# Kernel optimization log

Measured on AMD Instinct MI355X. Metric: run time of the kernel, lower is better.

The kernel has to match this reference:

```python
import jax, jax.numpy as jnp
import numpy as np

HIDDEN = 1024
INTER = 4096
N_EXPERTS = 8


def geglu(x, w1, w2, w3):
    # x: [N, C], w1/w2: [C, I], w3: [I, C]
    return (jax.nn.gelu(x @ w1, approximate=False) * (x @ w2)) @ w3


def setup_inputs() -> dict:
    key = jax.random.key(0)
    ks = jax.random.split(key, 8)
    s = 0.02
    x = jax.random.normal(ks[0], (2, 2048, HIDDEN), dtype=jnp.float32)
    w1s = jax.random.normal(ks[1], (HIDDEN, INTER), dtype=jnp.float32) * s
    w2s = jax.random.normal(ks[2], (HIDDEN, INTER), dtype=jnp.float32) * s
    w3s = jax.random.normal(ks[3], (INTER, HIDDEN), dtype=jnp.float32) * s
    W1 = jax.random.normal(ks[4], (N_EXPERTS, HIDDEN, INTER), dtype=jnp.float32) * s
    W2 = jax.random.normal(ks[5], (N_EXPERTS, HIDDEN, INTER), dtype=jnp.float32) * s
    W3 = jax.random.normal(ks[6], (N_EXPERTS, INTER, HIDDEN), dtype=jnp.float32) * s
    Wg = jax.random.normal(ks[7], (HIDDEN, N_EXPERTS), dtype=jnp.float32) * s
    return {"x": x, "w1s": w1s, "w2s": w2s, "w3s": w3s,
            "W1": W1, "W2": W2, "W3": W3, "Wg": Wg}


def reference(x, w1s, w2s, w3s, W1, W2, W3, Wg):
    B, T, C = x.shape
    xf = x.reshape(-1, C)  # [N, C]
    shared = geglu(xf, w1s, w2s, w3s)  # [N, C]
    logits = xf @ Wg  # [N, E]
    # top-1 of softmax == argmax of logits (softmax is monotone);
    # NOTE: original torch code does NOT multiply by the routing prob.
    idx = jnp.argmax(logits, axis=-1)  # [N]
    final = jnp.zeros_like(xf)
    for e in range(N_EXPERTS):  # small fixed expert count
        y = geglu(xf, W1[e], W2[e], W3[e])  # [N, C]
        final = final + jnp.where((idx == e)[:, None], y, 0.0)
    return (shared + final).reshape(B, T, C)
```

## Files before the change

### kernel.cpp

```cpp
#include <hip/hip_runtime.h>
#include <stdint.h>

#define HIDDEN 1024
#define INTER  4096
#define NTOK   4096
#define HROWS  (2*NTOK)
#define MAXB1  40
#define MAXB2  72
#define NMAT   27

typedef unsigned short u16;
typedef unsigned int   u32;
typedef __bf16  bf16x8 __attribute__((ext_vector_type(8)));
typedef float   f32x4  __attribute__((ext_vector_type(4)));
typedef u32     u32x4  __attribute__((ext_vector_type(4)));

#define WAITVM(N) asm volatile("s_waitcnt vmcnt(" #N ")" ::: "memory")

__device__ __forceinline__ void hard_barrier() {
  asm volatile("" ::: "memory");
  __builtin_amdgcn_s_barrier();
  asm volatile("" ::: "memory");
}

__device__ __forceinline__ u16 f2bf(float f) {
  u32 u = __float_as_uint(f);
  u32 r = u + 0x7FFFu + ((u >> 16) & 1u);
  return (u16)(r >> 16);
}

__device__ __forceinline__ u32 cvt_pk_bf16(float lo, float hi) {
  u32 r;
  asm("v_cvt_pk_bf16_f32 %0, %1, %2" : "=v"(r) : "v"(lo), "v"(hi));
  return r;
}

__device__ __forceinline__ void glds16(const void* g, void* l) {
  __builtin_amdgcn_global_load_lds(
      (const __attribute__((address_space(1))) void*)g,
      (__attribute__((address_space(3))) void*)l, 16, 0, 0);
}


__global__ void k_init(int* cnt, int* fill) {
  if (threadIdx.x < 8) { cnt[threadIdx.x] = 0; fill[threadIdx.x] = 0; }
}

__global__ __launch_bounds__(256) void k_gate(const float* __restrict__ x,
                                              const float* __restrict__ wg,
                                              int* __restrict__ idx,
                                              int* __restrict__ cnt) {
  int wave = threadIdx.x >> 6, lane = threadIdx.x & 63;
  int t = blockIdx.x * 4 + wave;
  if (t >= NTOK) return;
  float acc[8];
  #pragma unroll
  for (int e = 0; e < 8; ++e) acc[e] = 0.f;
  const float* xr = x + (size_t)t * HIDDEN;
  for (int c = lane; c < HIDDEN; c += 64) {
    float xv = xr[c];
    const float* wrow = wg + (size_t)c * 8;
    #pragma unroll
    for (int e = 0; e < 8; ++e) acc[e] += xv * wrow[e];
  }
  #pragma unroll
  for (int e = 0; e < 8; ++e)
    for (int s = 32; s; s >>= 1) acc[e] += __shfl_xor(acc[e], s);
  if (lane == 0) {
    int best = 0; float bv = acc[0];
    #pragma unroll
    for (int e = 1; e < 8; ++e) if (acc[e] > bv) { bv = acc[e]; best = e; }
    idx[t] = best;
    atomicAdd(&cnt[best], 1);
  }
}

__global__ void k_cvt(const float* __restrict__ x, u16* __restrict__ xb, int n4) {
  int i = blockIdx.x * blockDim.x + threadIdx.x;
  if (i >= n4) return;
  float4 v = ((const float4*)x)[i];
  ushort4 o;
  o.x = f2bf(v.x); o.y = f2bf(v.y); o.z = f2bf(v.z); o.w = f2bf(v.w);
  ((ushort4*)xb)[i] = o;
}

__global__ void k_table(const int* __restrict__ cnt, int* __restrict__ off,
                        int4* __restrict__ tab1, int* __restrict__ nblk1,
                        int4* __restrict__ tab2, int* __restrict__ nblk2) {
  if (threadIdx.x != 0 || blockIdx.x != 0) return;
  int o = 0;
  int offs[8];
  for (int e = 0; e < 8; ++e) { offs[e] = o; off[e] = o; o += cnt[e]; }
  int nb = 0;
  for (int m = 0; m < NTOK / 256; ++m)
    tab1[nb++] = make_int4(8, m * 256, 256, 0);
  for (int e = 0; e < 8; ++e)
    for (int j = 0; j * 256 < cnt[e]; ++j) {
      int rows = cnt[e] - j * 256; if (rows > 256) rows = 256;
      tab1[nb++] = make_int4(e, NTOK + offs[e] + j * 256, rows, offs[e] + j * 256);
    }
  *nblk1 = nb;
  nb = 0;
  for (int m = 0; m < NTOK / 128; ++m)
    tab2[nb++] = make_int4(8, m * 128, 128, 0);
  for (int e = 0; e < 8; ++e)
    for (int j = 0; j * 128 < cnt[e]; ++j) {
      int rows = cnt[e] - j * 128; if (rows > 128) rows = 128;
      tab2[nb++] = make_int4(e, NTOK + offs[e] + j * 128, rows, offs[e] + j * 128);
    }
  *nblk2 = nb;
}

__global__ void k_scatter(const int* __restrict__ idx, const int* __restrict__ off,
                          int* __restrict__ fill, int* __restrict__ perm) {
  int t = blockIdx.x * blockDim.x + threadIdx.x;
  if (t >= NTOK) return;
  int e = idx[t];
  int p = atomicAdd(&fill[e], 1);
  perm[off[e] + p] = t;
}


__global__ __launch_bounds__(256) void k_wcvt(
    const float* __restrict__ w1s, const float* __restrict__ w2s,
    const float* __restrict__ w3s, const float* __restrict__ W1,
    const float* __restrict__ W2,  const float* __restrict__ W3,
    u16* __restrict__ Wb)
{
  int bid = blockIdx.x;
  int m = bid >> 9, pair = bid & 511;
  const float* src; int N, Tp, kt, pp2;
  if (m < 18) {
    N = INTER; Tp = 32;
    int mm = (m < 9) ? m : m - 9;
    const float* sp = (m < 9) ? w1s : w2s;
    const float* ep = (m < 9) ? W1 : W2;
    src = (mm == 0) ? sp : ep + (size_t)(mm - 1) * HIDDEN * INTER;
    kt = pair >> 4; pp2 = pair & 15;
  } else {
    N = HIDDEN; Tp = 8;
    int mm = m - 18;
    src = (mm == 0) ? w3s : W3 + (size_t)(mm - 1) * INTER * HIDDEN;
    kt = pair >> 2; pp2 = pair & 3;
  }

  __shared__ float tileF[32 * 256];
  int tid = threadIdx.x;
  const float* in0 = src + (size_t)(kt * 32) * N + pp2 * 256;
  #pragma unroll
  for (int i = 0; i < 8; ++i) {
    int f = tid + 256 * i;
    int k = f >> 6, c4 = f & 63;
    *(float4*)&tileF[k * 256 + c4 * 4] = *(const float4*)(in0 + (size_t)k * N + c4 * 4);
  }
  __syncthreads();

  int p2 = tid >> 7, n = tid & 127;
  u16* outp = Wb + ((size_t)m * 1024 + kt * Tp + pp2 * 2 + p2) * 4096 + n * 32;
  #pragma unroll
  for (int s = 0; s < 4; ++s) {
    int k8 = s ^ ((n >> 1) & 3);
    const float* col = &tileF[(k8 * 8) * 256 + p2 * 128 + n];
    u32x4 pk;
    pk.x = cvt_pk_bf16(col[0],    col[256]);
    pk.y = cvt_pk_bf16(col[512],  col[768]);
    pk.z = cvt_pk_bf16(col[1024], col[1280]);
    pk.w = cvt_pk_bf16(col[1536], col[1792]);
    *(u32x4*)(outp + s * 8) = pk;
  }
}


__global__ __launch_bounds__(512, 2) void k_mlp1(
    const u16* __restrict__ xb, const u16* __restrict__ Wb,
    const int* __restrict__ perm, const int4* __restrict__ tab,
    const int* __restrict__ nblk, u16* __restrict__ Hbuf)
{
  int bx = blockIdx.x;
  if (bx >= *nblk) return;
  int4 te = tab[bx];
  int g = te.x, hrow0 = te.y, rows = te.z, pb = te.w;
  int m1 = (g == 8) ? 0 : 1 + g;
  int pp = blockIdx.y;
  int nbase = pp * 128;

  extern __shared__ __align__(16) char smem[];
  int tid = threadIdx.x;
  int w = tid >> 6, lane = tid & 63;
  int q = lane >> 4, rl = lane & 15;
  int mw = w >> 2, nw = w & 3;

  int tokj[2];
  #pragma unroll
  for (int j = 0; j < 2; ++j) {
    int r = w * 32 + j * 16 + (lane >> 2);
    int rc = (r < rows) ? r : (rows - 1);
    tokj[j] = (g == 8) ? (hrow0 + rc) : perm[pb + rc];
  }
  int gch = ((lane & 3) ^ ((lane >> 3) & 3)) * 16;

  const char* pB1 = (const char*)Wb + ((size_t)m1 * 1024 + pp) * 8192;
  const char* pB2 = (const char*)Wb + ((size_t)(m1 + 9) * 1024 + pp) * 8192;

  f32x4 acc1[8][2], acc2[8][2];
  f32x4 z = {0.f, 0.f, 0.f, 0.f};
  #pragma unroll
  for (int mi = 0; mi < 8; ++mi)
    #pragma unroll
    for (int ni = 0; ni < 2; ++ni) { acc1[mi][ni] = z; acc2[mi][ni] = z; }

  auto STAGE = [&](int t) {
    char* L = smem + (t & 3) * 32768;
    int k0 = t * 32;
    #pragma unroll
    for (int j = 0; j < 2; ++j) {
      const char* src = (const char*)xb + ((size_t)tokj[j] * HIDDEN + k0) * 2 + gch;
      glds16(src, L + w * 2048 + j * 1024);
    }
    glds16(pB1 + (size_t)t * 262144 + (tid << 4), L + 16384 + w * 1024);
    glds16(pB2 + (size_t)t * 262144 + (tid << 4), L + 24576 + w * 1024);
  };

  int co = (q ^ ((rl >> 1) & 3)) * 8;

  auto COMPUTE = [&](int t) {
    const u16* LA  = (const u16*)(smem + (t & 3) * 32768);
    const u16* LB1 = LA + 8192;
    const u16* LB2 = LA + 12288;
    bf16x8 af[8], b1[2], b2[2];
    #pragma unroll
    for (int mi = 0; mi < 8; ++mi)
      af[mi] = *(const bf16x8*)&LA[(mw * 128 + mi * 16 + rl) * 32 + co];
    #pragma unroll
    for (int ni = 0; ni < 2; ++ni) {
      int n = nw * 32 + ni * 16 + rl;
      b1[ni] = *(const bf16x8*)&LB1[n * 32 + co];
      b2[ni] = *(const bf16x8*)&LB2[n * 32 + co];
    }
    __builtin_amdgcn_s_setprio(1);
    #pragma unroll
    for (int mi = 0; mi < 8; ++mi)
      #pragma unroll
      for (int ni = 0; ni < 2; ++ni) {
        acc1[mi][ni] = __builtin_amdgcn_mfma_f32_16x16x32_bf16(af[mi], b1[ni], acc1[mi][ni], 0, 0, 0);
        acc2[mi][ni] = __builtin_amdgcn_mfma_f32_16x16x32_bf16(af[mi], b2[ni], acc2[mi][ni], 0, 0, 0);
      }
    __builtin_amdgcn_s_setprio(0);
  };

  const int NT = HIDDEN / 32;
  STAGE(0); STAGE(1); STAGE(2);
  for (int t = 0; t < NT; ++t) {
    if (t + 3 < NT) STAGE(t + 3);
    int rem = NT - 1 - t;
    if (rem >= 3)      WAITVM(12);
    else if (rem == 2) WAITVM(8);
    else if (rem == 1) WAITVM(4);
    else               WAITVM(0);
    hard_barrier();
    COMPUTE(t);
    hard_barrier();
  }

  #pragma unroll
  for (int mi = 0; mi < 8; ++mi) {
    #pragma unroll
    for (int j = 0; j < 4; ++j) {
      int r = mw * 128 + mi * 16 + q * 4 + j;
      if (r < rows) {
        size_t hb = (size_t)(hrow0 + r) * INTER + nbase + nw * 32;
        #pragma unroll
        for (int ni = 0; ni < 2; ++ni) {
          float h1 = acc1[mi][ni][j];
          float h2 = acc2[mi][ni][j];
          float ge = 0.5f * h1 * (1.0f + erff(h1 * 0.7071067811865476f));
          Hbuf[hb + ni * 16 + rl] = f2bf(ge * h2);
        }
      }
    }
  }
}


__global__ __launch_bounds__(512, 2) void k_mlp2(
    const u16* __restrict__ Hbuf, const u16* __restrict__ Wb,
    const int* __restrict__ perm, const int4* __restrict__ tab,
    const int* __restrict__ nblk, float* __restrict__ out,
    float* __restrict__ yexp)
{
  int bx = blockIdx.x;
  if (bx >= *nblk) return;
  int4 te = tab[bx];
  int g = te.x, hrow0 = te.y, rows = te.z, pb = te.w;
  int m3 = (g == 8) ? 18 : 19 + g;
  int pp2 = blockIdx.y;

  extern __shared__ __align__(16) char smem[];
  int tid = threadIdx.x;
  int w = tid >> 6, lane = tid & 63;
  int q = lane >> 4, rl = lane & 15;
  int mw = w >> 2, nw = w & 3;

  int rr = w * 16 + (lane >> 2);
  int rc = (rr < rows) ? rr : (rows - 1);
  int hr = hrow0 + rc;
  int gch = ((lane & 3) ^ ((lane >> 3) & 3)) * 16;

  const char* pB = (const char*)Wb + ((size_t)m3 * 1024 + pp2 * 2) * 8192;

  f32x4 acc[4][4];
  f32x4 z = {0.f, 0.f, 0.f, 0.f};
  #pragma unroll
  for (int mi = 0; mi < 4; ++mi)
    #pragma unroll
    for (int ni = 0; ni < 4; ++ni) acc[mi][ni] = z;

  auto STAGE = [&](int t) {
    char* L = smem + (t & 3) * 24576;
    int k0 = t * 32;
    const char* src = (const char*)Hbuf + ((size_t)hr * INTER + k0) * 2 + gch;
    glds16(src, L + w * 1024);
    #pragma unroll
    for (int j = 0; j < 2; ++j)
      glds16(pB + (size_t)t * 65536 + j * 8192 + (tid << 4), L + 8192 + j * 8192 + w * 1024);
  };

  int co = (q ^ ((rl >> 1) & 3)) * 8;

  auto COMPUTE = [&](int t) {
    const u16* LA = (const u16*)(smem + (t & 3) * 24576);
    const u16* LB = LA + 4096;
    bf16x8 af[4], bf[4];
    #pragma unroll
    for (int mi = 0; mi < 4; ++mi)
      af[mi] = *(const bf16x8*)&LA[(mw * 64 + mi * 16 + rl) * 32 + co];
    #pragma unroll
    for (int ni = 0; ni < 4; ++ni) {
      int n = nw * 64 + ni * 16 + rl;
      bf[ni] = *(const bf16x8*)&LB[n * 32 + co];
    }
    __builtin_amdgcn_s_setprio(1);
    #pragma unroll
    for (int mi = 0; mi < 4; ++mi)
      #pragma unroll
      for (int ni = 0; ni < 4; ++ni)
        acc[mi][ni] = __builtin_amdgcn_mfma_f32_16x16x32_bf16(af[mi], bf[ni], acc[mi][ni], 0, 0, 0);
    __builtin_amdgcn_s_setprio(0);
  };

  const int NT = INTER / 32;
  STAGE(0); STAGE(1); STAGE(2);
  for (int t = 0; t < NT; ++t) {
    if (t + 3 < NT) STAGE(t + 3);
    int rem = NT - 1 - t;
    if (rem >= 3)      WAITVM(9);
    else if (rem == 2) WAITVM(6);
    else if (rem == 1) WAITVM(3);
    else               WAITVM(0);
    hard_barrier();
    COMPUTE(t);
    hard_barrier();
  }

  float* dstb = (g == 8) ? out : yexp;
  #pragma unroll
  for (int mi = 0; mi < 4; ++mi) {
    #pragma unroll
    for (int j = 0; j < 4; ++j) {
      int r = mw * 64 + mi * 16 + q * 4 + j;
      if (r < rows) {
        int tok = (g == 8) ? (hrow0 + r) : perm[pb + r];
        size_t ob = (size_t)tok * HIDDEN + pp2 * 256 + nw * 64;
        #pragma unroll
        for (int ni = 0; ni < 4; ++ni)
          dstb[ob + ni * 16 + rl] = acc[mi][ni][j];
      }
    }
  }
}

__global__ void k_add(float* __restrict__ out, const float* __restrict__ yexp, int n4) {
  int i = blockIdx.x * blockDim.x + threadIdx.x;
  if (i >= n4) return;
  float4 a = ((const float4*)out)[i];
  float4 b = ((const float4*)yexp)[i];
  a.x += b.x; a.y += b.y; a.z += b.z; a.w += b.w;
  ((float4*)out)[i] = a;
}


extern "C" void kernel_launch(void* const* d_in, const int* in_sizes, int n_in,
                              void* d_out, int out_size, void* d_ws, size_t ws_size,
                              hipStream_t stream) {
  const float* x   = (const float*)d_in[0];
  const float* w1s = (const float*)d_in[1];
  const float* w2s = (const float*)d_in[2];
  const float* w3s = (const float*)d_in[3];
  const float* W1  = (const float*)d_in[4];
  const float* W2  = (const float*)d_in[5];
  const float* W3  = (const float*)d_in[6];
  const float* Wg  = (const float*)d_in[7];
  float* out = (float*)d_out;

  char* ws = (char*)d_ws;
  size_t o_xb   = 0;
  size_t o_H    = o_xb   + (size_t)NTOK * HIDDEN * 2;
  size_t o_yexp = o_H    + (size_t)HROWS * INTER * 2;
  size_t o_Wb   = o_yexp + (size_t)NTOK * HIDDEN * 4;
  size_t o_idx  = o_Wb   + (size_t)NMAT * 1024 * 8192;
  size_t o_perm = o_idx  + (size_t)NTOK * 4;
  size_t o_cnt  = o_perm + (size_t)NTOK * 4;
  size_t o_off  = o_cnt  + 32;
  size_t o_fill = o_off  + 32;
  size_t o_nb1  = o_fill + 32;
  size_t o_nb2  = o_nb1  + 32;
  size_t o_tab1 = o_nb2  + 32;
  size_t o_tab2 = o_tab1 + (size_t)MAXB1 * 16;
  size_t need   = o_tab2 + (size_t)MAXB2 * 16;
  if (ws_size < need) return;

  u16*  xb   = (u16*)(ws + o_xb);
  u16*  Hbuf = (u16*)(ws + o_H);
  float* yexp = (float*)(ws + o_yexp);
  u16*  Wb   = (u16*)(ws + o_Wb);
  int*  idx  = (int*)(ws + o_idx);
  int*  perm = (int*)(ws + o_perm);
  int*  cnt  = (int*)(ws + o_cnt);
  int*  off  = (int*)(ws + o_off);
  int*  fill = (int*)(ws + o_fill);
  int*  nblk1 = (int*)(ws + o_nb1);
  int*  nblk2 = (int*)(ws + o_nb2);
  int4* tab1 = (int4*)(ws + o_tab1);
  int4* tab2 = (int4*)(ws + o_tab2);

  k_init<<<1, 64, 0, stream>>>(cnt, fill);
  k_gate<<<NTOK / 4, 256, 0, stream>>>(x, Wg, idx, cnt);
  k_cvt<<<(NTOK * HIDDEN / 4) / 256, 256, 0, stream>>>(x, xb, NTOK * HIDDEN / 4);
  k_wcvt<<<NMAT * 512, 256, 0, stream>>>(w1s, w2s, w3s, W1, W2, W3, Wb);
  k_table<<<1, 1, 0, stream>>>(cnt, off, tab1, nblk1, tab2, nblk2);
  k_scatter<<<NTOK / 256, 256, 0, stream>>>(idx, off, fill, perm);
  k_mlp1<<<dim3(MAXB1, INTER / 128), 512, 131072, stream>>>(xb, Wb, perm, tab1, nblk1, Hbuf);
  k_mlp2<<<dim3(MAXB2, HIDDEN / 256), 512, 98304, stream>>>(Hbuf, Wb, perm, tab2, nblk2, out, yexp);
  k_add<<<(NTOK * HIDDEN / 4) / 256, 256, 0, stream>>>(out, yexp, NTOK * HIDDEN / 4);
}
```

Measured before the change: 561.7 us.

## Restructure GEMM main loops to wait once per iteration and interleave staged loads

Both GEMM kernels now wait at the end of each iteration for the next tile, not at the start. Each loop body issues its prefetch of tile t+3 after reading its LDS fragments. The first kernel also splits each K-step into two halves: A-tile loads go out during the first half of the MFMAs and B-tile loads during the second, with a barrier between them. This is meant to hide global-to-LDS latency better and to drop one barrier per iteration in the second GEMM. The added intra-iteration barrier in the first kernel and the tighter vmcnt accounting could add stalls if the counts are off.

```diff
diff --git a/kernel.cpp b/kernel.cpp
--- a/kernel.cpp
+++ b/kernel.cpp
@@ -209,7 +209,7 @@
     #pragma unroll
     for (int ni = 0; ni < 2; ++ni) { acc1[mi][ni] = z; acc2[mi][ni] = z; }
 
-  auto STAGE = [&](int t) {
+  auto STAGE_A = [&](int t) {
     char* L = smem + (t & 3) * 32768;
     int k0 = t * 32;
     #pragma unroll
@@ -217,19 +217,30 @@
       const char* src = (const char*)xb + ((size_t)tokj[j] * HIDDEN + k0) * 2 + gch;
       glds16(src, L + w * 2048 + j * 1024);
     }
+  };
+  auto STAGE_B = [&](int t) {
+    char* L = smem + (t & 3) * 32768;
     glds16(pB1 + (size_t)t * 262144 + (tid << 4), L + 16384 + w * 1024);
     glds16(pB2 + (size_t)t * 262144 + (tid << 4), L + 24576 + w * 1024);
   };
 
   int co = (q ^ ((rl >> 1) & 3)) * 8;
 
-  auto COMPUTE = [&](int t) {
+  const int NT = HIDDEN / 32;
+  STAGE_A(0); STAGE_B(0);
+  STAGE_A(1); STAGE_B(1);
+  STAGE_A(2); STAGE_B(2);
+  WAITVM(8);
+  hard_barrier();
+
+  for (int t = 0; t < NT; ++t) {
     const u16* LA  = (const u16*)(smem + (t & 3) * 32768);
     const u16* LB1 = LA + 8192;
     const u16* LB2 = LA + 12288;
     bf16x8 af[8], b1[2], b2[2];
-    #pragma unroll
-    for (int mi = 0; mi < 8; ++mi)
+
+    #pragma unroll
+    for (int mi = 0; mi < 4; ++mi)
       af[mi] = *(const bf16x8*)&LA[(mw * 128 + mi * 16 + rl) * 32 + co];
     #pragma unroll
     for (int ni = 0; ni < 2; ++ni) {
@@ -237,28 +248,37 @@
       b1[ni] = *(const bf16x8*)&LB1[n * 32 + co];
       b2[ni] = *(const bf16x8*)&LB2[n * 32 + co];
     }
+    if (t + 3 < NT) STAGE_A(t + 3);
     __builtin_amdgcn_s_setprio(1);
     #pragma unroll
-    for (int mi = 0; mi < 8; ++mi)
+    for (int mi = 0; mi < 4; ++mi)
       #pragma unroll
       for (int ni = 0; ni < 2; ++ni) {
         acc1[mi][ni] = __builtin_amdgcn_mfma_f32_16x16x32_bf16(af[mi], b1[ni], acc1[mi][ni], 0, 0, 0);
         acc2[mi][ni] = __builtin_amdgcn_mfma_f32_16x16x32_bf16(af[mi], b2[ni], acc2[mi][ni], 0, 0, 0);
       }
     __builtin_amdgcn_s_setprio(0);
-  };
-
-  const int NT = HIDDEN / 32;
-  STAGE(0); STAGE(1); STAGE(2);
-  for (int t = 0; t < NT; ++t) {
-    if (t + 3 < NT) STAGE(t + 3);
-    int rem = NT - 1 - t;
-    if (rem >= 3)      WAITVM(12);
-    else if (rem == 2) WAITVM(8);
-    else if (rem == 1) WAITVM(4);
-    else               WAITVM(0);
     hard_barrier();
-    COMPUTE(t);
+
+    #pragma unroll
+    for (int mi = 4; mi < 8; ++mi)
+      af[mi] = *(const bf16x8*)&LA[(mw * 128 + mi * 16 + rl) * 32 + co];
+    if (t + 3 < NT) STAGE_B(t + 3);
+    __builtin_amdgcn_s_setprio(1);
+    #pragma unroll
+    for (int mi = 4; mi < 8; ++mi)
+      #pragma unroll
+      for (int ni = 0; ni < 2; ++ni) {
+        acc1[mi][ni] = __builtin_amdgcn_mfma_f32_16x16x32_bf16(af[mi], b1[ni], acc1[mi][ni], 0, 0, 0);
+        acc2[mi][ni] = __builtin_amdgcn_mfma_f32_16x16x32_bf16(af[mi], b2[ni], acc2[mi][ni], 0, 0, 0);
+      }
+    __builtin_amdgcn_s_setprio(0);
+    {
+      int rem = NT - 1 - t;
+      if (rem >= 3)      WAITVM(8);
+      else if (rem == 2) WAITVM(4);
+      else if (rem == 1) WAITVM(0);
+    }
     hard_barrier();
   }
 
@@ -327,7 +347,12 @@
 
   int co = (q ^ ((rl >> 1) & 3)) * 8;
 
-  auto COMPUTE = [&](int t) {
+  const int NT = INTER / 32;
+  STAGE(0); STAGE(1); STAGE(2);
+  WAITVM(6);
+  hard_barrier();
+
+  for (int t = 0; t < NT; ++t) {
     const u16* LA = (const u16*)(smem + (t & 3) * 24576);
     const u16* LB = LA + 4096;
     bf16x8 af[4], bf[4];
@@ -339,6 +364,7 @@
       int n = nw * 64 + ni * 16 + rl;
       bf[ni] = *(const bf16x8*)&LB[n * 32 + co];
     }
+    if (t + 3 < NT) STAGE(t + 3);
     __builtin_amdgcn_s_setprio(1);
     #pragma unroll
     for (int mi = 0; mi < 4; ++mi)
@@ -346,19 +372,12 @@
       for (int ni = 0; ni < 4; ++ni)
         acc[mi][ni] = __builtin_amdgcn_mfma_f32_16x16x32_bf16(af[mi], bf[ni], acc[mi][ni], 0, 0, 0);
     __builtin_amdgcn_s_setprio(0);
-  };
-
-  const int NT = INTER / 32;
-  STAGE(0); STAGE(1); STAGE(2);
-  for (int t = 0; t < NT; ++t) {
-    if (t + 3 < NT) STAGE(t + 3);
-    int rem = NT - 1 - t;
-    if (rem >= 3)      WAITVM(9);
-    else if (rem == 2) WAITVM(6);
-    else if (rem == 1) WAITVM(3);
-    else               WAITVM(0);
-    hard_barrier();
-    COMPUTE(t);
+    {
+      int rem = NT - 1 - t;
+      if (rem >= 3)      WAITVM(6);
+      else if (rem == 2) WAITVM(3);
+      else if (rem == 1) WAITVM(0);
+    }
     hard_barrier();
   }
 
```

Result: faster. 538.2 us (-4.2%).

## Restructure GEMM main loops with unrolled ring buffer and split-phase prefetch

Applied to the files above, without the earlier changes.

Changes the packed bf16 weight layout so each N-panel's K-tiles are contiguous, letting the kernels advance weight pointers by a fixed stride. The MLP1 and MLP2 main loops are rewritten as a manually unrolled four-stage ring of macro tiles with precomputed LDS read pointers and incrementing global pointers, cutting address arithmetic and one barrier per iteration. In MLP1 the global-to-LDS prefetch issues are interleaved between two halves of the MFMA work, with an extra barrier in the middle. The hardcoded vmcnt waits and loop trip counts must match the tile counts exactly, so mistakes there would silently race on LDS.

```diff
diff --git a/kernel.cpp b/kernel.cpp
--- a/kernel.cpp
+++ b/kernel.cpp
@@ -129,16 +129,16 @@
 {
   int bid = blockIdx.x;
   int m = bid >> 9, pair = bid & 511;
-  const float* src; int N, Tp, kt, pp2;
+  const float* src; int N, nkt, kt, pp2;
   if (m < 18) {
-    N = INTER; Tp = 32;
+    N = INTER; nkt = 32;
     int mm = (m < 9) ? m : m - 9;
     const float* sp = (m < 9) ? w1s : w2s;
     const float* ep = (m < 9) ? W1 : W2;
     src = (mm == 0) ? sp : ep + (size_t)(mm - 1) * HIDDEN * INTER;
     kt = pair >> 4; pp2 = pair & 15;
   } else {
-    N = HIDDEN; Tp = 8;
+    N = HIDDEN; nkt = 128;
     int mm = m - 18;
     src = (mm == 0) ? w3s : W3 + (size_t)(mm - 1) * INTER * HIDDEN;
     kt = pair >> 2; pp2 = pair & 3;
@@ -156,7 +156,8 @@
   __syncthreads();
 
   int p2 = tid >> 7, n = tid & 127;
-  u16* outp = Wb + ((size_t)m * 1024 + kt * Tp + pp2 * 2 + p2) * 4096 + n * 32;
+  int pidx = m * 1024 + (pp2 * 2 + p2) * nkt + kt;
+  u16* outp = Wb + (size_t)pidx * 4096 + n * 32;
   #pragma unroll
   for (int s = 0; s < 4; ++s) {
     int k8 = s ^ ((n >> 1) & 3);
@@ -170,6 +171,56 @@
   }
 }
 
+
+#define MLP1_TILE(B, STG, WN)                                                        \
+  do {                                                                               \
+    const u16* LA = pAr  + (B) * 16384;                                              \
+    const u16* L1 = pBr1 + (B) * 16384;                                              \
+    const u16* L2 = pBr2 + (B) * 16384;                                              \
+    bf16x8 af[8], f1[2], f2[2];                                                      \
+    _Pragma("unroll")                                                                \
+    for (int mi = 0; mi < 4; ++mi) af[mi] = *(const bf16x8*)(LA + mi * 512);         \
+    _Pragma("unroll")                                                                \
+    for (int ni = 0; ni < 2; ++ni) {                                                 \
+      f1[ni] = *(const bf16x8*)(L1 + ni * 512);                                      \
+      f2[ni] = *(const bf16x8*)(L2 + ni * 512);                                      \
+    }                                                                                \
+    if (STG) {                                                                       \
+      char* Ld = smem + (((B) + 3) & 3) * 32768;                                     \
+      glds16(srcA0, Ld + w * 2048);                                                  \
+      glds16(srcA1, Ld + w * 2048 + 1024);                                           \
+      srcA0 += 64; srcA1 += 64;                                                      \
+    }                                                                                \
+    __builtin_amdgcn_s_setprio(1);                                                   \
+    _Pragma("unroll")                                                                \
+    for (int mi = 0; mi < 4; ++mi) {                                                 \
+      acc1[mi][0] = __builtin_amdgcn_mfma_f32_16x16x32_bf16(af[mi], f1[0], acc1[mi][0], 0, 0, 0); \
+      acc1[mi][1] = __builtin_amdgcn_mfma_f32_16x16x32_bf16(af[mi], f1[1], acc1[mi][1], 0, 0, 0); \
+      acc2[mi][0] = __builtin_amdgcn_mfma_f32_16x16x32_bf16(af[mi], f2[0], acc2[mi][0], 0, 0, 0); \
+      acc2[mi][1] = __builtin_amdgcn_mfma_f32_16x16x32_bf16(af[mi], f2[1], acc2[mi][1], 0, 0, 0); \
+    }                                                                                \
+    __builtin_amdgcn_s_setprio(0);                                                   \
+    hard_barrier();                                                                  \
+    _Pragma("unroll")                                                                \
+    for (int mi = 4; mi < 8; ++mi) af[mi] = *(const bf16x8*)(LA + mi * 512);         \
+    if (STG) {                                                                       \
+      char* Ld = smem + (((B) + 3) & 3) * 32768;                                     \
+      glds16(srcB1, Ld + 16384 + w * 1024);                                          \
+      glds16(srcB2, Ld + 24576 + w * 1024);                                          \
+      srcB1 += 8192; srcB2 += 8192;                                                  \
+    }                                                                                \
+    __builtin_amdgcn_s_setprio(1);                                                   \
+    _Pragma("unroll")                                                                \
+    for (int mi = 4; mi < 8; ++mi) {                                                 \
+      acc1[mi][0] = __builtin_amdgcn_mfma_f32_16x16x32_bf16(af[mi], f1[0], acc1[mi][0], 0, 0, 0); \
+      acc1[mi][1] = __builtin_amdgcn_mfma_f32_16x16x32_bf16(af[mi], f1[1], acc1[mi][1], 0, 0, 0); \
+      acc2[mi][0] = __builtin_amdgcn_mfma_f32_16x16x32_bf16(af[mi], f2[0], acc2[mi][0], 0, 0, 0); \
+      acc2[mi][1] = __builtin_amdgcn_mfma_f32_16x16x32_bf16(af[mi], f2[1], acc2[mi][1], 0, 0, 0); \
+    }                                                                                \
+    __builtin_amdgcn_s_setprio(0);                                                   \
+    WN;                                                                              \
+    hard_barrier();                                                                  \
+  } while (0)
 
 __global__ __launch_bounds__(512, 2) void k_mlp1(
     const u16* __restrict__ xb, const u16* __restrict__ Wb,
@@ -199,8 +250,15 @@
   }
   int gch = ((lane & 3) ^ ((lane >> 3) & 3)) * 16;
 
-  const char* pB1 = (const char*)Wb + ((size_t)m1 * 1024 + pp) * 8192;
-  const char* pB2 = (const char*)Wb + ((size_t)(m1 + 9) * 1024 + pp) * 8192;
+  const char* srcA0 = (const char*)xb + (size_t)tokj[0] * 2048 + gch;
+  const char* srcA1 = (const char*)xb + (size_t)tokj[1] * 2048 + gch;
+  const char* srcB1 = (const char*)Wb + ((size_t)m1 * 1024 + pp * 32) * 8192 + (tid << 4);
+  const char* srcB2 = (const char*)Wb + ((size_t)(m1 + 9) * 1024 + pp * 32) * 8192 + (tid << 4);
+
+  int co = (q ^ ((rl >> 1) & 3)) * 8;
+  const u16* pAr  = (const u16*)smem + (mw * 128 + rl) * 32 + co;
+  const u16* pBr1 = (const u16*)smem + 8192  + (nw * 32 + rl) * 32 + co;
+  const u16* pBr2 = (const u16*)smem + 12288 + (nw * 32 + rl) * 32 + co;
 
   f32x4 acc1[8][2], acc2[8][2];
   f32x4 z = {0.f, 0.f, 0.f, 0.f};
@@ -209,58 +267,29 @@
     #pragma unroll
     for (int ni = 0; ni < 2; ++ni) { acc1[mi][ni] = z; acc2[mi][ni] = z; }
 
-  auto STAGE = [&](int t) {
-    char* L = smem + (t & 3) * 32768;
-    int k0 = t * 32;
-    #pragma unroll
-    for (int j = 0; j < 2; ++j) {
-      const char* src = (const char*)xb + ((size_t)tokj[j] * HIDDEN + k0) * 2 + gch;
-      glds16(src, L + w * 2048 + j * 1024);
-    }
-    glds16(pB1 + (size_t)t * 262144 + (tid << 4), L + 16384 + w * 1024);
-    glds16(pB2 + (size_t)t * 262144 + (tid << 4), L + 24576 + w * 1024);
-  };
-
-  int co = (q ^ ((rl >> 1) & 3)) * 8;
-
-  auto COMPUTE = [&](int t) {
-    const u16* LA  = (const u16*)(smem + (t & 3) * 32768);
-    const u16* LB1 = LA + 8192;
-    const u16* LB2 = LA + 12288;
-    bf16x8 af[8], b1[2], b2[2];
-    #pragma unroll
-    for (int mi = 0; mi < 8; ++mi)
-      af[mi] = *(const bf16x8*)&LA[(mw * 128 + mi * 16 + rl) * 32 + co];
-    #pragma unroll
-    for (int ni = 0; ni < 2; ++ni) {
-      int n = nw * 32 + ni * 16 + rl;
-      b1[ni] = *(const bf16x8*)&LB1[n * 32 + co];
-      b2[ni] = *(const bf16x8*)&LB2[n * 32 + co];
-    }
-    __builtin_amdgcn_s_setprio(1);
-    #pragma unroll
-    for (int mi = 0; mi < 8; ++mi)
-      #pragma unroll
-      for (int ni = 0; ni < 2; ++ni) {
-        acc1[mi][ni] = __builtin_amdgcn_mfma_f32_16x16x32_bf16(af[mi], b1[ni], acc1[mi][ni], 0, 0, 0);
-        acc2[mi][ni] = __builtin_amdgcn_mfma_f32_16x16x32_bf16(af[mi], b2[ni], acc2[mi][ni], 0, 0, 0);
-      }
-    __builtin_amdgcn_s_setprio(0);
-  };
-
-  const int NT = HIDDEN / 32;
-  STAGE(0); STAGE(1); STAGE(2);
-  for (int t = 0; t < NT; ++t) {
-    if (t + 3 < NT) STAGE(t + 3);
-    int rem = NT - 1 - t;
-    if (rem >= 3)      WAITVM(12);
-    else if (rem == 2) WAITVM(8);
-    else if (rem == 1) WAITVM(4);
-    else               WAITVM(0);
-    hard_barrier();
-    COMPUTE(t);
-    hard_barrier();
-  }
+  #pragma unroll
+  for (int p = 0; p < 3; ++p) {
+    char* Ld = smem + p * 32768;
+    glds16(srcA0, Ld + w * 2048);
+    glds16(srcA1, Ld + w * 2048 + 1024);
+    srcA0 += 64; srcA1 += 64;
+    glds16(srcB1, Ld + 16384 + w * 1024);
+    glds16(srcB2, Ld + 24576 + w * 1024);
+    srcB1 += 8192; srcB2 += 8192;
+  }
+  WAITVM(8);
+  hard_barrier();
+
+  for (int t0 = 0; t0 < 28; t0 += 4) {
+    MLP1_TILE(0, 1, WAITVM(8));
+    MLP1_TILE(1, 1, WAITVM(8));
+    MLP1_TILE(2, 1, WAITVM(8));
+    MLP1_TILE(3, 1, WAITVM(8));
+  }
+  MLP1_TILE(0, 1, WAITVM(8));
+  MLP1_TILE(1, 0, WAITVM(4));
+  MLP1_TILE(2, 0, WAITVM(0));
+  MLP1_TILE(3, 0, (void)0);
 
   #pragma unroll
   for (int mi = 0; mi < 8; ++mi) {
@@ -282,6 +311,32 @@
 }
 
 
+#define MLP2_TILE(B, STG, WN)                                                        \
+  do {                                                                               \
+    const u16* LA = pAr + (B) * 12288;                                               \
+    const u16* LB = pBr + (B) * 12288;                                               \
+    bf16x8 af[4], bf[4];                                                             \
+    _Pragma("unroll")                                                                \
+    for (int mi = 0; mi < 4; ++mi) af[mi] = *(const bf16x8*)(LA + mi * 512);         \
+    _Pragma("unroll")                                                                \
+    for (int ni = 0; ni < 4; ++ni) bf[ni] = *(const bf16x8*)(LB + ni * 512);         \
+    if (STG) {                                                                       \
+      char* Ld = smem + (((B) + 3) & 3) * 24576;                                     \
+      glds16(srcA0, Ld + w * 1024);              srcA0 += 64;                        \
+      glds16(srcB0, Ld + 8192 + w * 1024);       srcB0 += 8192;                      \
+      glds16(srcB1, Ld + 16384 + w * 1024);      srcB1 += 8192;                      \
+    }                                                                                \
+    __builtin_amdgcn_s_setprio(1);                                                   \
+    _Pragma("unroll")                                                                \
+    for (int mi = 0; mi < 4; ++mi)                                                   \
+      _Pragma("unroll")                                                              \
+      for (int ni = 0; ni < 4; ++ni)                                                 \
+        acc[mi][ni] = __builtin_amdgcn_mfma_f32_16x16x32_bf16(af[mi], bf[ni], acc[mi][ni], 0, 0, 0); \
+    __builtin_amdgcn_s_setprio(0);                                                   \
+    WN;                                                                              \
+    hard_barrier();                                                                  \
+  } while (0)
+
 __global__ __launch_bounds__(512, 2) void k_mlp2(
     const u16* __restrict__ Hbuf, const u16* __restrict__ Wb,
     const int* __restrict__ perm, const int4* __restrict__ tab,
@@ -306,7 +361,13 @@
   int hr = hrow0 + rc;
   int gch = ((lane & 3) ^ ((lane >> 3) & 3)) * 16;
 
-  const char* pB = (const char*)Wb + ((size_t)m3 * 1024 + pp2 * 2) * 8192;
+  const char* srcA0 = (const char*)Hbuf + (size_t)hr * (INTER * 2) + gch;
+  const char* srcB0 = (const char*)Wb + ((size_t)m3 * 1024 + (pp2 * 2) * 128) * 8192 + (tid << 4);
+  const char* srcB1 = (const char*)Wb + ((size_t)m3 * 1024 + (pp2 * 2 + 1) * 128) * 8192 + (tid << 4);
+
+  int co = (q ^ ((rl >> 1) & 3)) * 8;
+  const u16* pAr = (const u16*)smem + (mw * 64 + rl) * 32 + co;
+  const u16* pBr = (const u16*)smem + 4096 + (nw * 64 + rl) * 32 + co;
 
   f32x4 acc[4][4];
   f32x4 z = {0.f, 0.f, 0.f, 0.f};
@@ -315,52 +376,26 @@
     #pragma unroll
     for (int ni = 0; ni < 4; ++ni) acc[mi][ni] = z;
 
-  auto STAGE = [&](int t) {
-    char* L = smem + (t & 3) * 24576;
-    int k0 = t * 32;
-    const char* src = (const char*)Hbuf + ((size_t)hr * INTER + k0) * 2 + gch;
-    glds16(src, L + w * 1024);
-    #pragma unroll
-    for (int j = 0; j < 2; ++j)
-      glds16(pB + (size_t)t * 65536 + j * 8192 + (tid << 4), L + 8192 + j * 8192 + w * 1024);
-  };
-
-  int co = (q ^ ((rl >> 1) & 3)) * 8;
-
-  auto COMPUTE = [&](int t) {
-    const u16* LA = (const u16*)(smem + (t & 3) * 24576);
-    const u16* LB = LA + 4096;
-    bf16x8 af[4], bf[4];
-    #pragma unroll
-    for (int mi = 0; mi < 4; ++mi)
-      af[mi] = *(const bf16x8*)&LA[(mw * 64 + mi * 16 + rl) * 32 + co];
-    #pragma unroll
-    for (int ni = 0; ni < 4; ++ni) {
-      int n = nw * 64 + ni * 16 + rl;
-      bf[ni] = *(const bf16x8*)&LB[n * 32 + co];
-    }
-    __builtin_amdgcn_s_setprio(1);
-    #pragma unroll
-    for (int mi = 0; mi < 4; ++mi)
-      #pragma unroll
-      for (int ni = 0; ni < 4; ++ni)
-        acc[mi][ni] = __builtin_amdgcn_mfma_f32_16x16x32_bf16(af[mi], bf[ni], acc[mi][ni], 0, 0, 0);
-    __builtin_amdgcn_s_setprio(0);
-  };
-
-  const int NT = INTER / 32;
-  STAGE(0); STAGE(1); STAGE(2);
-  for (int t = 0; t < NT; ++t) {
-    if (t + 3 < NT) STAGE(t + 3);
-    int rem = NT - 1 - t;
-    if (rem >= 3)      WAITVM(9);
-    else if (rem == 2) WAITVM(6);
-    else if (rem == 1) WAITVM(3);
-    else               WAITVM(0);
-    hard_barrier();
-    COMPUTE(t);
-    hard_barrier();
-  }
+  #pragma unroll
+  for (int p = 0; p < 3; ++p) {
+    char* Ld = smem + p * 24576;
+    glds16(srcA0, Ld + w * 1024);          srcA0 += 64;
+    glds16(srcB0, Ld + 8192 + w * 1024);   srcB0 += 8192;
+    glds16(srcB1, Ld + 16384 + w * 1024);  srcB1 += 8192;
+  }
+  WAITVM(6);
+  hard_barrier();
+
+  for (int t0 = 0; t0 < 124; t0 += 4) {
+    MLP2_TILE(0, 1, WAITVM(6));
+    MLP2_TILE(1, 1, WAITVM(6));
+    MLP2_TILE(2, 1, WAITVM(6));
+    MLP2_TILE(3, 1, WAITVM(6));
+  }
+  MLP2_TILE(0, 1, WAITVM(6));
+  MLP2_TILE(1, 0, WAITVM(3));
+  MLP2_TILE(2, 0, WAITVM(0));
+  MLP2_TILE(3, 0, (void)0);
 
   float* dstb = (g == 8) ? out : yexp;
   #pragma unroll
```

After: 524.0 us. 6.7% less time.
